# Kernel optimization log

Measured on AMD Instinct MI355X. Metric: run time of the kernel, lower is better.

The kernel has to match this reference:

```python
import jax, jax.numpy as jnp
import numpy as np

N_NODES, IN_F, HIDDEN, N_EDGES, N_TRAIN, N_CLASS = 50000, 64, 512, 160000, 80000, 7
BN_EPS = 1e-5

def _lin(k, fin, fout):
    return jax.random.normal(k, (fin, fout), jnp.float32) * 0.05, jnp.zeros((fout,), jnp.float32)

def setup_inputs() -> dict:
    key = jax.random.key(0)
    ks = jax.random.split(key, 12)
    x = jax.random.normal(ks[0], (N_NODES, IN_F), jnp.float32)
    edge_index = jax.random.randint(ks[1], (2, N_EDGES), 0, N_NODES, jnp.int32)
    train_edge_id = jax.random.randint(ks[2], (N_TRAIN,), 0, N_EDGES, jnp.int32)
    W1, b1 = _lin(ks[3], IN_F, HIDDEN)
    W2, b2 = _lin(ks[4], HIDDEN, HIDDEN)
    W3, b3 = _lin(ks[5], HIDDEN, HIDDEN)
    W4, b4 = _lin(ks[6], HIDDEN, HIDDEN)
    lin1_W, lin1_b = _lin(ks[7], HIDDEN, HIDDEN)
    lin2_W, lin2_b = _lin(ks[8], HIDDEN, HIDDEN)
    fc2_W, fc2_b = _lin(ks[9], HIDDEN, N_CLASS)
    ones = jnp.ones((HIDDEN,), jnp.float32); zeros = jnp.zeros((HIDDEN,), jnp.float32)
    return dict(x=x, edge_index=edge_index, train_edge_id=train_edge_id,
                W1=W1, b1=b1, W2=W2, b2=b2, W3=W3, b3=b3,
                bn1_g=ones, bn1_b=zeros, bn1_m=zeros, bn1_v=ones, eps1=jnp.float32(0.0),
                W4=W4, b4=b4, bn2_g=ones, bn2_b=zeros, bn2_m=zeros, bn2_v=ones, eps2=jnp.float32(0.0),
                lin1_W=lin1_W, lin1_b=lin1_b, lin2_W=lin2_W, lin2_b=lin2_b,
                fc2_W=fc2_W, fc2_b=fc2_b)

def _gin_agg(h, src, dst, eps):
    # PyG GINConv: (1+eps)*x_i + sum_{j in N(i)} x_j, messages flow src->dst
    agg = jax.ops.segment_sum(h[src], dst, num_segments=N_NODES)
    return (1.0 + eps) * h + agg

def _bn(h, g, b, m, v):
    return (h - m) * jax.lax.rsqrt(v + BN_EPS) * g + b

def reference(x, edge_index, train_edge_id, W1, b1, W2, b2, W3, b3,
              bn1_g, bn1_b, bn1_m, bn1_v, eps1,
              W4, b4, bn2_g, bn2_b, bn2_m, bn2_v, eps2,
              lin1_W, lin1_b, lin2_W, lin2_b, fc2_W, fc2_b):
    src, dst = edge_index[0], edge_index[1]
    h = _gin_agg(x, src, dst, eps1)
    h = jax.nn.relu(h @ W1 + b1)
    h = jax.nn.relu(h @ W2 + b2)
    h = jax.nn.relu(h @ W3 + b3)
    h = _bn(h, bn1_g, bn1_b, bn1_m, bn1_v)
    # gin_convs[0]: agg -> Linear+ReLU -> BN
    h = _gin_agg(h, src, dst, eps2)
    h = jax.nn.relu(h @ W4 + b4)
    h = _bn(h, bn2_g, bn2_b, bn2_m, bn2_v)
    # node MLP head (dropout = identity in eval)
    h = jax.nn.relu(h @ lin1_W + lin1_b)
    h = h @ lin2_W + lin2_b
    # edge-gather fusion (feature_fusion=None -> elementwise mul)
    node_id = edge_index[:, train_edge_id]  # [2, T]
    x1 = h[node_id[0]]
    x2 = h[node_id[1]]
    return (x1 * x2) @ fc2_W + fc2_b  # [T, class_num]
```

## Files before the change

### kernel.cpp

```cpp
#include <hip/hip_runtime.h>

#define N_NODES 50000
#define MPAD    50048
#define IN_F    64
#define HIDDEN  512
#define N_EDGES 160000
#define N_TRAIN 80000
#define N_CLASS 7
#define BN_EPS  1e-5f

#define MT      (MPAD / 128)
#define NT      4
#define FULLGRP ((MT / 8) * 32)
#define NBLK    ((N_NODES + 255) / 256)

#define NT4     2
#define FULLG4  ((MT / 8) * 16)
#define NG4     (MT * NT4)

typedef short  bf16x8 __attribute__((ext_vector_type(8)));
typedef float  f32x4  __attribute__((ext_vector_type(4)));
typedef unsigned short ushort_t;

__device__ __forceinline__ ushort_t f2b(float v) {
    union { float f; unsigned int u; } c; c.f = v;
    unsigned int x = c.u;
    unsigned int r = (x + 0x7FFFu + ((x >> 16) & 1u)) >> 16;
    return (ushort_t)r;
}
__device__ __forceinline__ float b2f(ushort_t b) {
    union { unsigned int u; float f; } c; c.u = ((unsigned int)b) << 16;
    return c.f;
}

__device__ __forceinline__ void async_copy16(const void* g, void* l) {
    __builtin_amdgcn_global_load_lds(
        (const __attribute__((address_space(1))) void*)g,
        (__attribute__((address_space(3))) void*)l, 16, 0, 0);
}

__global__ void zero_kernel(int* __restrict__ p, int n) {
    int i = blockIdx.x * blockDim.x + threadIdx.x;
    if (i < n) p[i] = 0;
}

__global__ void hist_kernel(const int* __restrict__ ei, int* __restrict__ deg) {
    int e = blockIdx.x * blockDim.x + threadIdx.x;
    if (e >= N_EDGES) return;
    atomicAdd(&deg[ei[N_EDGES + e]], 1);
}

__global__ __launch_bounds__(256) void blocksum_kernel(const int* __restrict__ deg,
                                                       int* __restrict__ bsum) {
    __shared__ int s[256];
    int i = blockIdx.x * 256 + threadIdx.x;
    s[threadIdx.x] = (i < N_NODES) ? deg[i] : 0;
    __syncthreads();
    for (int off = 128; off > 0; off >>= 1) {
        if (threadIdx.x < off) s[threadIdx.x] += s[threadIdx.x + off];
        __syncthreads();
    }
    if (threadIdx.x == 0) bsum[blockIdx.x] = s[0];
}

__global__ __launch_bounds__(256) void scanbsum_kernel(const int* __restrict__ bsum,
                                                       int* __restrict__ boff) {
    __shared__ int s[256];
    int tid = threadIdx.x;
    s[tid] = (tid < NBLK) ? bsum[tid] : 0;
    __syncthreads();
    for (int off = 1; off < 256; off <<= 1) {
        int t = (tid >= off) ? s[tid - off] : 0;
        __syncthreads();
        s[tid] += t;
        __syncthreads();
    }
    if (tid < NBLK) boff[tid] = (tid == 0) ? 0 : s[tid - 1];
}

__global__ __launch_bounds__(256) void rowptr_kernel(const int* __restrict__ deg,
                                                     const int* __restrict__ boff,
                                                     int* __restrict__ rowptr,
                                                     int* __restrict__ cursor) {
    __shared__ int s[256];
    int tid = threadIdx.x;
    int i = blockIdx.x * 256 + tid;
    int d = (i < N_NODES) ? deg[i] : 0;
    s[tid] = d;
    __syncthreads();
    for (int off = 1; off < 256; off <<= 1) {
        int t = (tid >= off) ? s[tid - off] : 0;
        __syncthreads();
        s[tid] += t;
        __syncthreads();
    }
    int incl = s[tid] + boff[blockIdx.x];
    if (i < N_NODES) {
        rowptr[i + 1] = incl;
        cursor[i] = incl - d;
    }
    if (i == 0) rowptr[0] = 0;
}

__global__ void scatter_kernel(const int* __restrict__ ei,
                               int* __restrict__ cursor, int* __restrict__ adj) {
    int e = blockIdx.x * blockDim.x + threadIdx.x;
    if (e >= N_EDGES) return;
    int src = ei[e], dst = ei[N_EDGES + e];
    int pos = atomicAdd(&cursor[dst], 1);
    adj[pos] = src;
}

__global__ __launch_bounds__(256) void gather64_kernel(
    const float* __restrict__ x, const int* __restrict__ rowptr,
    const int* __restrict__ adj, const float* __restrict__ epsp,
    ushort_t* __restrict__ hi, ushort_t* __restrict__ lo) {
    int wave = threadIdx.x >> 6, lane = threadIdx.x & 63;
    int n = blockIdx.x * 4 + wave;
    if (n >= N_NODES) return;
    float s = 1.0f + *epsp;
    float sum = s * x[(size_t)n * IN_F + lane];
    int beg = rowptr[n], end = rowptr[n + 1];
    for (int k = beg; k < end; k++) {
        sum += x[(size_t)adj[k] * IN_F + lane];
    }
    ushort_t hb = f2b(sum);
    ushort_t lb = f2b(sum - b2f(hb));
    hi[(size_t)n * IN_F + lane] = hb;
    lo[(size_t)n * IN_F + lane] = lb;
}

__global__ __launch_bounds__(256) void gather512_kernel(
    const float* __restrict__ h, const int* __restrict__ rowptr,
    const int* __restrict__ adj, const float* __restrict__ epsp,
    ushort_t* __restrict__ hi, ushort_t* __restrict__ lo) {
    int wave = threadIdx.x >> 6, lane = threadIdx.x & 63;
    int n = blockIdx.x * 2 + (wave >> 1);
    if (n >= N_NODES) return;
    float s = 1.0f + *epsp;
    const int f = (wave & 1) * 256 + lane * 4;
    float4 a = *(const float4*)&h[(size_t)n * HIDDEN + f];
    float sum[4] = {s * a.x, s * a.y, s * a.z, s * a.w};
    int beg = rowptr[n], end = rowptr[n + 1];
    for (int k = beg; k < end; k++) {
        float4 b = *(const float4*)&h[(size_t)adj[k] * HIDDEN + f];
        sum[0] += b.x; sum[1] += b.y; sum[2] += b.z; sum[3] += b.w;
    }
    ushort_t h4[4], l4[4];
#pragma unroll
    for (int j = 0; j < 4; j++) {
        h4[j] = f2b(sum[j]);
        l4[j] = f2b(sum[j] - b2f(h4[j]));
    }
    *(ushort4*)&hi[(size_t)n * HIDDEN + f] = make_ushort4(h4[0], h4[1], h4[2], h4[3]);
    *(ushort4*)&lo[(size_t)n * HIDDEN + f] = make_ushort4(l4[0], l4[1], l4[2], l4[3]);
}

__global__ void wtrans_all_kernel(const float* __restrict__ w0,
                                  const float* __restrict__ w1,
                                  const float* __restrict__ w2,
                                  const float* __restrict__ w3,
                                  const float* __restrict__ w4,
                                  const float* __restrict__ w5,
                                  ushort_t* __restrict__ Wp) {
    const size_t WSMALL = (size_t)HIDDEN * IN_F;
    const size_t WBIG   = (size_t)HIDDEN * HIDDEN;
    int z = blockIdx.z;
    const float* W = (z == 0) ? w0 : (z == 1) ? w1 : (z == 2) ? w2
                   : (z == 3) ? w3 : (z == 4) ? w4 : w5;
    int K = (z == 0) ? IN_F : HIDDEN;
    size_t off_h = (z == 0) ? 0 : 2 * WSMALL + (size_t)(z - 1) * 2 * WBIG;
    ushort_t* Whi = Wp + off_h;
    ushort_t* Wlo = Whi + ((z == 0) ? WSMALL : WBIG);

    __shared__ float t[32][33];
    int tx = threadIdx.x & 31, ty = threadIdx.x >> 5;
    int nb = blockIdx.x * 32, kb = blockIdx.y * 32;
    if (kb >= K) return;
#pragma unroll
    for (int i = 0; i < 4; i++) {
        int k = kb + ty + i * 8;
        t[ty + i * 8][tx] = W[(size_t)k * HIDDEN + nb + tx];
    }
    __syncthreads();
#pragma unroll
    for (int i = 0; i < 4; i++) {
        int n = nb + ty + i * 8;
        int k = kb + tx;
        float v = t[tx][ty + i * 8];
        ushort_t hb = f2b(v);
        ushort_t lb = f2b(v - b2f(hb));
        Whi[(size_t)n * K + k] = hb;
        Wlo[(size_t)n * K + k] = lb;
    }
}

__global__ __launch_bounds__(256, 2) void gemm_split128x256_kernel(
    const ushort_t* __restrict__ Ahi, const ushort_t* __restrict__ Alo,
    const ushort_t* __restrict__ Bhi, const ushort_t* __restrict__ Blo,
    const float* __restrict__ bias,
    float* __restrict__ Cf, ushort_t* __restrict__ Chi, ushort_t* __restrict__ Clo,
    int mode,
    const float* __restrict__ bn_g, const float* __restrict__ bn_b,
    const float* __restrict__ bn_m, const float* __restrict__ bn_v) {
    const int K = HIDDEN;
    __shared__ ushort_t As_h[128 * 32];
    __shared__ ushort_t As_l[128 * 32];
    __shared__ ushort_t Bs_h[256 * 32];
    __shared__ ushort_t Bs_l[256 * 32];

    const int tid  = threadIdx.x;
    const int wave = tid >> 6, lane = tid & 63;
    const int quad = lane >> 4, r = lane & 15;

    int idx = blockIdx.x, m_t, n_t;
    if (idx < FULLG4) {
        m_t = (idx >> 4) * 8 + (idx & 7);
        n_t = (idx >> 3) & 1;
    } else {
        int t2 = idx - FULLG4;
        m_t = 384 + (t2 >> 1);
        n_t = t2 & 1;
    }
    const int m0 = m_t * 128, n0 = n_t * 256;

    const f32x4 vzero = {0.f, 0.f, 0.f, 0.f};
    f32x4 acc[8][4];
#pragma unroll
    for (int i = 0; i < 8; i++)
#pragma unroll
        for (int j = 0; j < 4; j++) acc[i][j] = vzero;

    const int srow = lane >> 2;
    const int scol = (((lane & 3) + ((srow >> 1) & 3)) & 3) * 8;
    const int csw  = ((quad - ((r >> 1) & 3)) & 3) * 8;

    for (int k0 = 0; k0 < K; k0 += 32) {
        __syncthreads();
#pragma unroll
        for (int tt = 0; tt < 2; tt++) {
            int base = wave * 32 + tt * 16;
            int rr = base + srow;
            int lba = base * 32;
            size_t ga = (size_t)(m0 + rr) * K + k0 + scol;
            async_copy16(Ahi + ga, &As_h[lba]);
            async_copy16(Alo + ga, &As_l[lba]);
        }
#pragma unroll
        for (int tt = 0; tt < 4; tt++) {
            int base = wave * 64 + tt * 16;
            int rr = base + srow;
            int lbb = base * 32;
            size_t gb = (size_t)(n0 + rr) * K + k0 + scol;
            async_copy16(Bhi + gb, &Bs_h[lbb]);
            async_copy16(Blo + gb, &Bs_l[lbb]);
        }
        __syncthreads();

        bf16x8 bh[4], bl[4];
#pragma unroll
        for (int j = 0; j < 4; j++) {
            int bofs = (wave * 64 + j * 16 + r) * 32 + csw;
            bh[j] = *(const bf16x8*)&Bs_h[bofs];
            bl[j] = *(const bf16x8*)&Bs_l[bofs];
        }
#pragma unroll
        for (int ih = 0; ih < 2; ih++) {
            bf16x8 ah[4], al[4];
#pragma unroll
            for (int i = 0; i < 4; i++) {
                int aofs = (ih * 64 + i * 16 + r) * 32 + csw;
                ah[i] = *(const bf16x8*)&As_h[aofs];
                al[i] = *(const bf16x8*)&As_l[aofs];
            }
#pragma unroll
            for (int i = 0; i < 4; i++)
#pragma unroll
                for (int j = 0; j < 4; j++) {
                    int ii = ih * 4 + i;
                    acc[ii][j] = __builtin_amdgcn_mfma_f32_16x16x32_bf16(ah[i], bh[j], acc[ii][j], 0, 0, 0);
                    acc[ii][j] = __builtin_amdgcn_mfma_f32_16x16x32_bf16(ah[i], bl[j], acc[ii][j], 0, 0, 0);
                    acc[ii][j] = __builtin_amdgcn_mfma_f32_16x16x32_bf16(al[i], bh[j], acc[ii][j], 0, 0, 0);
                }
        }
    }

    float bia[4], sc[4], sh[4];
#pragma unroll
    for (int j = 0; j < 4; j++) {
        int col = n0 + wave * 64 + j * 16 + r;
        bia[j] = bias[col];
        if (mode == 2) {
            float g = bn_g[col], bb = bn_b[col], mm = bn_m[col], vv = bn_v[col];
            sc[j] = g * rsqrtf(vv + BN_EPS);
            sh[j] = bb - mm * sc[j];
        } else { sc[j] = 1.f; sh[j] = 0.f; }
    }
#pragma unroll
    for (int ii = 0; ii < 8; ii++) {
#pragma unroll
        for (int rg = 0; rg < 4; rg++) {
            int row = m0 + ii * 16 + quad * 4 + rg;
            if (row >= N_NODES) continue;
#pragma unroll
            for (int j = 0; j < 4; j++) {
                int col = n0 + wave * 64 + j * 16 + r;
                float v = acc[ii][j][rg] + bia[j];
                if (mode >= 1) v = fmaxf(v, 0.f);
                if (mode == 2) v = v * sc[j] + sh[j];
                size_t oix = (size_t)row * HIDDEN + col;
                if (Cf) {
                    Cf[oix] = v;
                } else {
                    ushort_t hb = f2b(v);
                    ushort_t lb = f2b(v - b2f(hb));
                    Chi[oix] = hb;
                    Clo[oix] = lb;
                }
            }
        }
    }
}

__global__ __launch_bounds__(256) void gemm_k64_kernel(
    const ushort_t* __restrict__ Ahi, const ushort_t* __restrict__ Alo,
    const ushort_t* __restrict__ Bhi, const ushort_t* __restrict__ Blo,
    const float* __restrict__ bias,
    ushort_t* __restrict__ Chi, ushort_t* __restrict__ Clo) {
    const int K = 64;
    __shared__ ushort_t As_h[128 * 64];
    __shared__ ushort_t As_l[128 * 64];
    __shared__ ushort_t Bs_h[128 * 64];
    __shared__ ushort_t Bs_l[128 * 64];

    const int tid  = threadIdx.x;
    const int wave = tid >> 6, lane = tid & 63;
    const int wm = wave >> 1, wn = wave & 1;
    const int quad = lane >> 4, r = lane & 15;

    int idx = blockIdx.x, m_t, n_t;
    if (idx < FULLGRP) {
        m_t = (idx >> 5) * 8 + (idx & 7);
        n_t = (idx >> 3) & 3;
    } else {
        int t = idx - FULLGRP;
        m_t = (FULLGRP >> 2) + (t >> 2);
        n_t = t & 3;
    }
    const int m0 = m_t * 128, n0 = n_t * 128;

    const int srow8 = lane >> 3;
    const int sc8   = (((lane & 7) - srow8) & 7) * 8;
#pragma unroll
    for (int t = 0; t < 4; t++) {
        int base = wave * 32 + t * 8;
        int rr = base + srow8;
        int lbase = base * 64;
        size_t ga = (size_t)(m0 + rr) * K + sc8;
        size_t gb = (size_t)(n0 + rr) * K + sc8;
        async_copy16(Ahi + ga, &As_h[lbase]);
        async_copy16(Alo + ga, &As_l[lbase]);
        async_copy16(Bhi + gb, &Bs_h[lbase]);
        async_copy16(Blo + gb, &Bs_l[lbase]);
    }
    __syncthreads();

    const f32x4 vzero = {0.f, 0.f, 0.f, 0.f};
    f32x4 acc[4][4];
#pragma unroll
    for (int i = 0; i < 4; i++)
#pragma unroll
        for (int j = 0; j < 4; j++) acc[i][j] = vzero;

#pragma unroll
    for (int ks = 0; ks < 2; ks++) {
        bf16x8 ah[4], al[4], bh[4], bl[4];
#pragma unroll
        for (int i = 0; i < 4; i++) {
            int ra = wm * 64 + i * 16 + r;
            int rb = wn * 64 + i * 16 + r;
            int ca = ((quad + ks * 4 + (ra & 7)) & 7) * 8;
            int cb = ((quad + ks * 4 + (rb & 7)) & 7) * 8;
            ah[i] = *(const bf16x8*)&As_h[ra * 64 + ca];
            al[i] = *(const bf16x8*)&As_l[ra * 64 + ca];
            bh[i] = *(const bf16x8*)&Bs_h[rb * 64 + cb];
            bl[i] = *(const bf16x8*)&Bs_l[rb * 64 + cb];
        }
#pragma unroll
        for (int i = 0; i < 4; i++)
#pragma unroll
            for (int j = 0; j < 4; j++) {
                acc[i][j] = __builtin_amdgcn_mfma_f32_16x16x32_bf16(ah[i], bh[j], acc[i][j], 0, 0, 0);
                acc[i][j] = __builtin_amdgcn_mfma_f32_16x16x32_bf16(ah[i], bl[j], acc[i][j], 0, 0, 0);
                acc[i][j] = __builtin_amdgcn_mfma_f32_16x16x32_bf16(al[i], bh[j], acc[i][j], 0, 0, 0);
            }
    }

    float bia[4];
#pragma unroll
    for (int j = 0; j < 4; j++) bia[j] = bias[n0 + wn * 64 + j * 16 + r];
#pragma unroll
    for (int i = 0; i < 4; i++) {
#pragma unroll
        for (int rg = 0; rg < 4; rg++) {
            int row = m0 + wm * 64 + i * 16 + quad * 4 + rg;
            if (row >= N_NODES) continue;
#pragma unroll
            for (int j = 0; j < 4; j++) {
                int col = n0 + wn * 64 + j * 16 + r;
                float v = fmaxf(acc[i][j][rg] + bia[j], 0.f);
                size_t oix = (size_t)row * HIDDEN + col;
                ushort_t hb = f2b(v);
                ushort_t lb = f2b(v - b2f(hb));
                Chi[oix] = hb;
                Clo[oix] = lb;
            }
        }
    }
}

__global__ __launch_bounds__(256) void fc2_kernel(
    const float* __restrict__ h, const int* __restrict__ ei,
    const int* __restrict__ teid, const float* __restrict__ W,
    const float* __restrict__ bias, float* __restrict__ out) {
    __shared__ float Ws[HIDDEN * N_CLASS];
    __shared__ float bs[N_CLASS];
    for (int i = threadIdx.x; i < HIDDEN * N_CLASS; i += blockDim.x) Ws[i] = W[i];
    if (threadIdx.x < N_CLASS) bs[threadIdx.x] = bias[threadIdx.x];
    __syncthreads();

    int wave = threadIdx.x >> 6;
    int lane = threadIdx.x & 63;
    int t = blockIdx.x * 4 + wave;
    if (t >= N_TRAIN) return;

    int e = teid[t];
    int a = ei[e];
    int b = ei[N_EDGES + e];
    const float* xa = h + (size_t)a * HIDDEN;
    const float* xb = h + (size_t)b * HIDDEN;

    float acc[N_CLASS];
#pragma unroll
    for (int c = 0; c < N_CLASS; c++) acc[c] = 0.f;

    int j0 = lane * 8;
    float4 a0 = *(const float4*)&xa[j0];
    float4 a1 = *(const float4*)&xa[j0 + 4];
    float4 b0 = *(const float4*)&xb[j0];
    float4 b1 = *(const float4*)&xb[j0 + 4];
    float p[8] = {a0.x * b0.x, a0.y * b0.y, a0.z * b0.z, a0.w * b0.w,
                  a1.x * b1.x, a1.y * b1.y, a1.z * b1.z, a1.w * b1.w};
#pragma unroll
    for (int jj = 0; jj < 8; jj++) {
        const float* wrow = &Ws[(j0 + jj) * N_CLASS];
#pragma unroll
        for (int c = 0; c < N_CLASS; c++) acc[c] = fmaf(p[jj], wrow[c], acc[c]);
    }
#pragma unroll
    for (int c = 0; c < N_CLASS; c++) {
        float v = acc[c];
        for (int off = 32; off > 0; off >>= 1) v += __shfl_down(v, off, 64);
        if (lane == 0) out[(size_t)t * N_CLASS + c] = v + bs[c];
    }
}

extern "C" void kernel_launch(void* const* d_in, const int* in_sizes, int n_in,
                              void* d_out, int out_size, void* d_ws, size_t ws_size,
                              hipStream_t stream) {
    const float* x      = (const float*)d_in[0];
    const int*   ei     = (const int*)d_in[1];
    const int*   teid   = (const int*)d_in[2];
    const float* W1     = (const float*)d_in[3];
    const float* b1     = (const float*)d_in[4];
    const float* W2     = (const float*)d_in[5];
    const float* b2     = (const float*)d_in[6];
    const float* W3     = (const float*)d_in[7];
    const float* b3     = (const float*)d_in[8];
    const float* bn1_g  = (const float*)d_in[9];
    const float* bn1_b  = (const float*)d_in[10];
    const float* bn1_m  = (const float*)d_in[11];
    const float* bn1_v  = (const float*)d_in[12];
    const float* eps1   = (const float*)d_in[13];
    const float* W4     = (const float*)d_in[14];
    const float* b4     = (const float*)d_in[15];
    const float* bn2_g  = (const float*)d_in[16];
    const float* bn2_b  = (const float*)d_in[17];
    const float* bn2_m  = (const float*)d_in[18];
    const float* bn2_v  = (const float*)d_in[19];
    const float* eps2   = (const float*)d_in[20];
    const float* lin1_W = (const float*)d_in[21];
    const float* lin1_b = (const float*)d_in[22];
    const float* lin2_W = (const float*)d_in[23];
    const float* lin2_b = (const float*)d_in[24];
    const float* fc2_W  = (const float*)d_in[25];
    const float* fc2_b  = (const float*)d_in[26];

    const size_t PLANE   = (size_t)MPAD * HIDDEN;
    const size_t PLANE64 = (size_t)MPAD * IN_F;

    ushort_t* R0h = (ushort_t*)d_ws;
    ushort_t* R0l = R0h + PLANE;
    ushort_t* R1h = R0l + PLANE;
    ushort_t* R1l = R1h + PLANE;

    const size_t WSMALL = (size_t)HIDDEN * IN_F;
    const size_t WBIG   = (size_t)HIDDEN * HIDDEN;
    ushort_t* Wp   = R1l + PLANE;
    ushort_t* Wt1h = Wp;            ushort_t* Wt1l = Wt1h + WSMALL;
    ushort_t* Wt2h = Wt1l + WSMALL; ushort_t* Wt2l = Wt2h + WBIG;
    ushort_t* Wt3h = Wt2l + WBIG;   ushort_t* Wt3l = Wt3h + WBIG;
    ushort_t* Wt4h = Wt3l + WBIG;   ushort_t* Wt4l = Wt4h + WBIG;
    ushort_t* Wt5h = Wt4l + WBIG;   ushort_t* Wt5l = Wt5h + WBIG;
    ushort_t* Wt6h = Wt5l + WBIG;   ushort_t* Wt6l = Wt6h + WBIG;

    int* deg    = (int*)(Wt6l + WBIG);
    int* cursor = deg + N_NODES;
    int* rowptr = cursor + N_NODES;
    int* bsum   = rowptr + (N_NODES + 1);
    int* boff   = bsum + NBLK;
    int* adj    = boff + NBLK;

    float* F32_R0 = (float*)R0h;
    ushort_t* H0h = R1h;
    ushort_t* H0l = R1h + PLANE64;

    zero_kernel<<<(N_NODES + 255) / 256, 256, 0, stream>>>(deg, N_NODES);
    hist_kernel<<<(N_EDGES + 255) / 256, 256, 0, stream>>>(ei, deg);
    blocksum_kernel<<<NBLK, 256, 0, stream>>>(deg, bsum);
    scanbsum_kernel<<<1, 256, 0, stream>>>(bsum, boff);
    rowptr_kernel<<<NBLK, 256, 0, stream>>>(deg, boff, rowptr, cursor);
    scatter_kernel<<<(N_EDGES + 255) / 256, 256, 0, stream>>>(ei, cursor, adj);

    wtrans_all_kernel<<<dim3(16, 16, 6), 256, 0, stream>>>(W1, W2, W3, W4,
                                                           lin1_W, lin2_W, Wp);

    const int ngrid = MT * NT;
    int nwb = (N_NODES + 3) / 4;

    gather64_kernel<<<nwb, 256, 0, stream>>>(x, rowptr, adj, eps1, H0h, H0l);

    gemm_k64_kernel<<<ngrid, 256, 0, stream>>>(H0h, H0l, Wt1h, Wt1l, b1, R0h, R0l);
    gemm_split128x256_kernel<<<NG4, 256, 0, stream>>>(R0h, R0l, Wt2h, Wt2l, b2,
        nullptr, R1h, R1l, 1, nullptr, nullptr, nullptr, nullptr);
    gemm_split128x256_kernel<<<NG4, 256, 0, stream>>>(R1h, R1l, Wt3h, Wt3l, b3,
        F32_R0, nullptr, nullptr, 2, bn1_g, bn1_b, bn1_m, bn1_v);

    gather512_kernel<<<(N_NODES + 1) / 2, 256, 0, stream>>>(F32_R0, rowptr, adj,
                                                            eps2, R1h, R1l);

    gemm_split128x256_kernel<<<NG4, 256, 0, stream>>>(R1h, R1l, Wt4h, Wt4l, b4,
        nullptr, R0h, R0l, 2, bn2_g, bn2_b, bn2_m, bn2_v);
    gemm_split128x256_kernel<<<NG4, 256, 0, stream>>>(R0h, R0l, Wt5h, Wt5l, lin1_b,
        nullptr, R1h, R1l, 1, nullptr, nullptr, nullptr, nullptr);
    gemm_split128x256_kernel<<<NG4, 256, 0, stream>>>(R1h, R1l, Wt6h, Wt6l, lin2_b,
        F32_R0, nullptr, nullptr, 0, nullptr, nullptr, nullptr, nullptr);

    fc2_kernel<<<(N_TRAIN + 3) / 4, 256, 0, stream>>>(F32_R0, ei, teid, fc2_W, fc2_b,
                                                      (float*)d_out);
}
```

Baseline: 843.1 us.

## Swizzle GEMM block IDs across XCDs and batch adjacency loads in 512-wide gather

Both GEMM kernels now remap blockIdx through an XCD-aware swizzle. Consecutive logical tiles, which share A or B panels, then land on the same XCD and can reuse its L2. The 512-feature gather loads up to 64 neighbor indices per wave in one coalesced read and hands them out with shuffles. It also software-pipelines the row loads one step ahead. This adds shuffle overhead per neighbor, and the swizzle changes tile scheduling order across the grid.

```diff
diff --git a/kernel.cpp b/kernel.cpp
--- a/kernel.cpp
+++ b/kernel.cpp
@@ -12,6 +12,7 @@
 #define MT      (MPAD / 128)
 #define NT      4
 #define FULLGRP ((MT / 8) * 32)
+#define NGK     (MT * NT)
 #define NBLK    ((N_NODES + 255) / 256)
 
 #define NT4     2
@@ -37,6 +38,13 @@
     __builtin_amdgcn_global_load_lds(
         (const __attribute__((address_space(1))) void*)g,
         (__attribute__((address_space(3))) void*)l, 16, 0, 0);
+}
+
+template<int NWG>
+__device__ __forceinline__ int xcd_swizzle(int orig) {
+    const int q = NWG >> 3, r = NWG & 7;
+    int xcd = orig & 7, slot = orig >> 3;
+    return (xcd < r ? xcd * (q + 1) : r * (q + 1) + (xcd - r) * q) + slot;
 }
 
 __global__ void zero_kernel(int* __restrict__ p, int n) {
@@ -142,9 +150,18 @@
     float4 a = *(const float4*)&h[(size_t)n * HIDDEN + f];
     float sum[4] = {s * a.x, s * a.y, s * a.z, s * a.w};
     int beg = rowptr[n], end = rowptr[n + 1];
-    for (int k = beg; k < end; k++) {
-        float4 b = *(const float4*)&h[(size_t)adj[k] * HIDDEN + f];
-        sum[0] += b.x; sum[1] += b.y; sum[2] += b.z; sum[3] += b.w;
+    for (int cb = beg; cb < end; cb += 64) {
+        int myadj = (cb + lane < end) ? adj[cb + lane] : 0;
+        int cnt = min(end - cb, 64);
+        int nb0 = __shfl(myadj, 0, 64);
+        float4 b0 = *(const float4*)&h[(size_t)nb0 * HIDDEN + f];
+        for (int k = 1; k < cnt; k++) {
+            int nb1 = __shfl(myadj, k, 64);
+            float4 b1 = *(const float4*)&h[(size_t)nb1 * HIDDEN + f];
+            sum[0] += b0.x; sum[1] += b0.y; sum[2] += b0.z; sum[3] += b0.w;
+            b0 = b1;
+        }
+        sum[0] += b0.x; sum[1] += b0.y; sum[2] += b0.z; sum[3] += b0.w;
     }
     ushort_t h4[4], l4[4];
 #pragma unroll
@@ -213,7 +230,8 @@
     const int wave = tid >> 6, lane = tid & 63;
     const int quad = lane >> 4, r = lane & 15;
 
-    int idx = blockIdx.x, m_t, n_t;
+    int idx = xcd_swizzle<NG4>(blockIdx.x);
+    int m_t, n_t;
     if (idx < FULLG4) {
         m_t = (idx >> 4) * 8 + (idx & 7);
         n_t = (idx >> 3) & 1;
@@ -338,7 +356,8 @@
     const int wm = wave >> 1, wn = wave & 1;
     const int quad = lane >> 4, r = lane & 15;
 
-    int idx = blockIdx.x, m_t, n_t;
+    int idx = xcd_swizzle<NGK>(blockIdx.x);
+    int m_t, n_t;
     if (idx < FULLGRP) {
         m_t = (idx >> 5) * 8 + (idx & 7);
         n_t = (idx >> 3) & 3;
@@ -535,12 +554,11 @@
     wtrans_all_kernel<<<dim3(16, 16, 6), 256, 0, stream>>>(W1, W2, W3, W4,
                                                            lin1_W, lin2_W, Wp);
 
-    const int ngrid = MT * NT;
     int nwb = (N_NODES + 3) / 4;
 
     gather64_kernel<<<nwb, 256, 0, stream>>>(x, rowptr, adj, eps1, H0h, H0l);
 
-    gemm_k64_kernel<<<ngrid, 256, 0, stream>>>(H0h, H0l, Wt1h, Wt1l, b1, R0h, R0l);
+    gemm_k64_kernel<<<NGK, 256, 0, stream>>>(H0h, H0l, Wt1h, Wt1l, b1, R0h, R0l);
     gemm_split128x256_kernel<<<NG4, 256, 0, stream>>>(R0h, R0l, Wt2h, Wt2l, b2,
         nullptr, R1h, R1l, 1, nullptr, nullptr, nullptr, nullptr);
     gemm_split128x256_kernel<<<NG4, 256, 0, stream>>>(R1h, R1l, Wt3h, Wt3l, b3,
```

New measurement: 859.4 us. No clear change (+1.9%).

## Load B fragments directly from global memory and add XCD-aware block swizzle

Applied to the files above, without the earlier changes.

The split-bf16 GEMM no longer stages the weight (B) tile through LDS. Each wave now reads its bf16x8 B fragments straight from global memory, which is possible because each wave owns a disjoint 64-column slice of B. Block indices are also remapped so that consecutive tiles land on the same XCD, aiming for better L2 reuse of A and B. This halves LDS use and removes B async copies, but puts uncoalesced, latency-exposed global loads inside the MFMA loop, relying on L2 and cache hits for the small weight matrices.

```diff
diff --git a/kernel.cpp b/kernel.cpp
--- a/kernel.cpp
+++ b/kernel.cpp
@@ -12,6 +12,7 @@
 #define MT      (MPAD / 128)
 #define NT      4
 #define FULLGRP ((MT / 8) * 32)
+#define NGK     (MT * NT)
 #define NBLK    ((N_NODES + 255) / 256)
 
 #define NT4     2
@@ -37,6 +38,13 @@
     __builtin_amdgcn_global_load_lds(
         (const __attribute__((address_space(1))) void*)g,
         (__attribute__((address_space(3))) void*)l, 16, 0, 0);
+}
+
+template<int NWG>
+__device__ __forceinline__ int xcd_swizzle(int orig) {
+    const int q = NWG >> 3, r = NWG & 7;
+    int xcd = orig & 7, slot = orig >> 3;
+    return (xcd < r ? xcd * (q + 1) : r * (q + 1) + (xcd - r) * q) + slot;
 }
 
 __global__ void zero_kernel(int* __restrict__ p, int n) {
@@ -206,14 +214,13 @@
     const int K = HIDDEN;
     __shared__ ushort_t As_h[128 * 32];
     __shared__ ushort_t As_l[128 * 32];
-    __shared__ ushort_t Bs_h[256 * 32];
-    __shared__ ushort_t Bs_l[256 * 32];
 
     const int tid  = threadIdx.x;
     const int wave = tid >> 6, lane = tid & 63;
     const int quad = lane >> 4, r = lane & 15;
 
-    int idx = blockIdx.x, m_t, n_t;
+    int idx = xcd_swizzle<NG4>(blockIdx.x);
+    int m_t, n_t;
     if (idx < FULLG4) {
         m_t = (idx >> 4) * 8 + (idx & 7);
         n_t = (idx >> 3) & 1;
@@ -234,6 +241,13 @@
     const int srow = lane >> 2;
     const int scol = (((lane & 3) + ((srow >> 1) & 3)) & 3) * 8;
     const int csw  = ((quad - ((r >> 1) & 3)) & 3) * 8;
+
+    size_t bbase[4];
+#pragma unroll
+    for (int j = 0; j < 4; j++) {
+        int col = n0 + wave * 64 + j * 16 + r;
+        bbase[j] = (size_t)col * K + quad * 8;
+    }
 
     for (int k0 = 0; k0 < K; k0 += 32) {
         __syncthreads();
@@ -246,23 +260,13 @@
             async_copy16(Ahi + ga, &As_h[lba]);
             async_copy16(Alo + ga, &As_l[lba]);
         }
-#pragma unroll
-        for (int tt = 0; tt < 4; tt++) {
-            int base = wave * 64 + tt * 16;
-            int rr = base + srow;
-            int lbb = base * 32;
-            size_t gb = (size_t)(n0 + rr) * K + k0 + scol;
-            async_copy16(Bhi + gb, &Bs_h[lbb]);
-            async_copy16(Blo + gb, &Bs_l[lbb]);
-        }
         __syncthreads();
 
         bf16x8 bh[4], bl[4];
 #pragma unroll
         for (int j = 0; j < 4; j++) {
-            int bofs = (wave * 64 + j * 16 + r) * 32 + csw;
-            bh[j] = *(const bf16x8*)&Bs_h[bofs];
-            bl[j] = *(const bf16x8*)&Bs_l[bofs];
+            bh[j] = *(const bf16x8*)&Bhi[bbase[j] + k0];
+            bl[j] = *(const bf16x8*)&Blo[bbase[j] + k0];
         }
 #pragma unroll
         for (int ih = 0; ih < 2; ih++) {
@@ -535,12 +539,11 @@
     wtrans_all_kernel<<<dim3(16, 16, 6), 256, 0, stream>>>(W1, W2, W3, W4,
                                                            lin1_W, lin2_W, Wp);
 
-    const int ngrid = MT * NT;
     int nwb = (N_NODES + 3) / 4;
 
     gather64_kernel<<<nwb, 256, 0, stream>>>(x, rowptr, adj, eps1, H0h, H0l);
 
-    gemm_k64_kernel<<<ngrid, 256, 0, stream>>>(H0h, H0l, Wt1h, Wt1l, b1, R0h, R0l);
+    gemm_k64_kernel<<<NGK, 256, 0, stream>>>(H0h, H0l, Wt1h, Wt1l, b1, R0h, R0l);
     gemm_split128x256_kernel<<<NG4, 256, 0, stream>>>(R0h, R0l, Wt2h, Wt2l, b2,
         nullptr, R1h, R1l, 1, nullptr, nullptr, nullptr, nullptr);
     gemm_split128x256_kernel<<<NG4, 256, 0, stream>>>(R1h, R1l, Wt3h, Wt3l, b3,
```

Result: slower. 908.6 us (+7.8%).
